# Kernel optimization log

Measured on AMD Instinct MI355X. Metric: run time of the kernel, lower is better.

Reference implementation:

```python
import jax, jax.numpy as jnp
import numpy as np

H, D = 4, 64          # n_heads, feats_per_head (hidden_size = H*D = 256)
NEG_SLOPE = 0.2       # DGL GATv2Conv default negative_slope

N_GT, N_UBS, N_AG = 100000, 20000, 20000
E_SEEN, E_NEAR = 320000, 160000
F_GT, F_UBS, F_AG = 8, 8, 16
HID = H * D


def _linear_params(key, fan_in, fan_out):
    kw, kb = jax.random.split(key)
    s = 1.0 / np.sqrt(fan_in)
    W = jax.random.uniform(kw, (fan_in, fan_out), jnp.float32, -s, s)
    b = jax.random.uniform(kb, (fan_out,), jnp.float32, -s, s)
    return W, b


def setup_inputs() -> dict:
    key = jax.random.key(0)
    ks = jax.random.split(key, 16)
    inp = {
        'x_gt': jax.random.normal(ks[0], (N_GT, F_GT), jnp.float32),
        'x_ubs': jax.random.normal(ks[1], (N_UBS, F_UBS), jnp.float32),
        'x_agent': jax.random.normal(ks[2], (N_AG, F_AG), jnp.float32),
        'seen_src': jax.random.randint(ks[3], (E_SEEN,), 0, N_GT, jnp.int32),
        'seen_dst': jax.random.randint(ks[4], (E_SEEN,), 0, N_AG, jnp.int32),
        'near_src': jax.random.randint(ks[5], (E_NEAR,), 0, N_UBS, jnp.int32),
        'near_dst': jax.random.randint(ks[6], (E_NEAR,), 0, N_AG, jnp.int32),
    }
    # GATv2Conv 'seen': (gt -> agent)
    inp['Ws_seen'], inp['bs_seen'] = _linear_params(ks[7], F_GT, HID)
    inp['Wd_seen'], inp['bd_seen'] = _linear_params(ks[8], F_AG, HID)
    inp['attn_seen'] = jax.random.normal(ks[9], (H, D), jnp.float32) * 0.1
    inp['Wr_seen'], inp['br_seen'] = _linear_params(ks[10], F_AG, HID)
    # GATv2Conv 'near': (ubs -> agent)
    inp['Ws_near'], inp['bs_near'] = _linear_params(ks[11], F_UBS, HID)
    inp['Wd_near'], inp['bd_near'] = _linear_params(ks[12], F_AG, HID)
    inp['attn_near'] = jax.random.normal(ks[13], (H, D), jnp.float32) * 0.1
    inp['Wr_near'], inp['br_near'] = _linear_params(ks[14], F_AG, HID)
    # aggregation MLP: Linear(2*HID, HID) + ReLU
    inp['W_aggr'], inp['b_aggr'] = _linear_params(ks[15], 2 * HID, HID)
    return inp


def _gatv2(h_src, h_dst, src, dst, Ws, bs, Wd, bd, attn, Wr, br, n_dst):
    # DGL GATv2Conv, bipartite, residual=True, allow_zero_in_degree, ReLU activation
    fs = (h_src @ Ws + bs).reshape(-1, H, D)   # [Ns,H,D]
    fd = (h_dst @ Wd + bd).reshape(-1, H, D)   # [Nd,H,D]
    e = jax.nn.leaky_relu(fs[src] + fd[dst], NEG_SLOPE)     # [E,H,D]
    scores = jnp.einsum('ehd,hd->eh', e, attn)              # [E,H]
    # edge softmax over incoming edges of each dst node
    m = jax.ops.segment_max(scores, dst, num_segments=n_dst)
    m = jnp.where(jnp.isfinite(m), m, 0.0)                  # zero-in-degree guard
    ex = jnp.exp(scores - m[dst])
    denom = jax.ops.segment_sum(ex, dst, num_segments=n_dst)
    alpha = ex / denom[dst]                                 # [E,H]
    rst = jax.ops.segment_sum(alpha[:, :, None] * fs[src], dst, num_segments=n_dst)
    rst = rst + (h_dst @ Wr + br).reshape(-1, H, D)         # residual
    return jax.nn.relu(rst).reshape(n_dst, H * D)


def reference(x_gt, x_ubs, x_agent, seen_src, seen_dst, near_src, near_dst,
              Ws_seen, bs_seen, Wd_seen, bd_seen, attn_seen, Wr_seen, br_seen,
              Ws_near, bs_near, Wd_near, bd_near, attn_near, Wr_near, br_near,
              W_aggr, b_aggr):
    n_ag = x_agent.shape[0]
    x1 = _gatv2(x_gt, x_agent, seen_src, seen_dst,
                Ws_seen, bs_seen, Wd_seen, bd_seen, attn_seen, Wr_seen, br_seen, n_ag)
    x2 = _gatv2(x_ubs, x_agent, near_src, near_dst,
                Ws_near, bs_near, Wd_near, bd_near, attn_near, Wr_near, br_near, n_ag)
    x_out = jnp.concatenate((x1, x2), axis=1)               # [N_ag, 2*HID]
    return jax.nn.relu(x_out @ W_aggr + b_aggr)             # [N_ag, HID]
```

## Files before the change

### kernel.cpp

```cpp
#include <hip/hip_runtime.h>
#include <math.h>

#define NEG 0.2f

typedef short bf16x8 __attribute__((ext_vector_type(8)));
typedef float f32x4  __attribute__((ext_vector_type(4)));
typedef float f32x2  __attribute__((ext_vector_type(2)));

static __device__ __forceinline__ void fma4(float4& d, float s, const float4 w) {
    d.x = fmaf(s, w.x, d.x); d.y = fmaf(s, w.y, d.y);
    d.z = fmaf(s, w.z, d.z); d.w = fmaf(s, w.w, d.w);
}
static __device__ __forceinline__ f32x2 pkfma(f32x2 a, f32x2 b, f32x2 c) {
    return __builtin_elementwise_fma(a, b, c);
}
static __device__ __forceinline__ f32x2 splat2(float x) { return (f32x2){x, x}; }

static __device__ __forceinline__ unsigned short f2bf(float f) {
    unsigned int x = __float_as_uint(f);
    unsigned int r = (x + 0x7FFFu + ((x >> 16) & 1u)) >> 16;
    return (unsigned short)r;
}
static __device__ __forceinline__ float rlane(float v, int l) {
    return __int_as_float(__builtin_amdgcn_readlane(__float_as_int(v), l));
}

#define DPP_ADD(x, ctrl) \
    ((x) + __int_as_float(__builtin_amdgcn_update_dpp( \
        __float_as_int(x), __float_as_int(x), (ctrl), 0xF, 0xF, true)))
static __device__ __forceinline__ float rowsum16(float v) {
    v = DPP_ADD(v, 0xB1);
    v = DPP_ADD(v, 0x4E);
    v = DPP_ADD(v, 0x141);
    v = DPP_ADD(v, 0x140);
    return v;
}

__global__ void k_hist_wt(const int* __restrict__ dst_s, int Es,
                          const int* __restrict__ dst_n, int En,
                          int* __restrict__ deg_s, int* __restrict__ deg_n,
                          const float* __restrict__ W, unsigned short* __restrict__ Wt) {
    int i = blockIdx.x * 256 + threadIdx.x;
    if (i < Es) atomicAdd(&deg_s[dst_s[i]], 1);
    int j = i - Es;
    if (j >= 0 && j < En) atomicAdd(&deg_n[dst_n[j]], 1);
    if (i < 512 * 256) {
        int k = i >> 8, n = i & 255;
        Wt[(size_t)n * 512 + k] = f2bf(W[i]);
    }
}

__global__ __launch_bounds__(1024) void k_scan2(int* a, int na, int* b, int nb) {
    int* p = (blockIdx.x == 0) ? a : b;
    int n  = (blockIdx.x == 0) ? na : nb;
    __shared__ int sums[1024];
    int t = threadIdx.x;
    int C = (n + 1023) >> 10;
    int base = t * C;
    int s = 0;
    for (int j = 0; j < C; ++j) { int i = base + j; if (i < n) s += p[i]; }
    sums[t] = s;
    __syncthreads();
    for (int off = 1; off < 1024; off <<= 1) {
        int v = (t >= off) ? sums[t - off] : 0;
        __syncthreads();
        sums[t] += v;
        __syncthreads();
    }
    int run = (t == 0) ? 0 : sums[t - 1];
    for (int j = 0; j < C; ++j) {
        int i = base + j;
        if (i < n) { int v = p[i]; p[i] = run; run += v; }
    }
}

__global__ void k_scatter(const int* __restrict__ src_s, const int* __restrict__ dst_s, int Es,
                          const int* __restrict__ src_n, const int* __restrict__ dst_n, int En,
                          int* __restrict__ cur_s, int* __restrict__ cur_n,
                          int* __restrict__ csr_s, int* __restrict__ csr_n) {
    int i = blockIdx.x * 256 + threadIdx.x;
    if (i < Es) {
        int pos = atomicAdd(&cur_s[dst_s[i]], 1);
        csr_s[pos] = src_s[i];
    }
    int j = i - Es;
    if (j >= 0 && j < En) {
        int pos = atomicAdd(&cur_n[dst_n[j]], 1);
        csr_n[pos] = src_n[j];
    }
}

__global__ __launch_bounds__(256) void k_gat(
    const float* __restrict__ xsrc_s, const int* __restrict__ pfx_s, const int* __restrict__ csr_s,
    const float* __restrict__ Ws_s, const float* __restrict__ bs_s,
    const float* __restrict__ Wd_s, const float* __restrict__ bd_s,
    const float* __restrict__ at_s,
    const float* __restrict__ Wr_s, const float* __restrict__ br_s,
    const float* __restrict__ xsrc_n, const int* __restrict__ pfx_n, const int* __restrict__ csr_n,
    const float* __restrict__ Ws_n, const float* __restrict__ bs_n,
    const float* __restrict__ Wd_n, const float* __restrict__ bd_n,
    const float* __restrict__ at_n,
    const float* __restrict__ Wr_n, const float* __restrict__ br_n,
    const float* __restrict__ x_ag,
    unsigned short* __restrict__ xcat, int n_dst, int gNs)
{
    const bool seen = (int)blockIdx.x < gNs;
    const float* x_src = seen ? xsrc_s : xsrc_n;
    const int*   pfx   = seen ? pfx_s  : pfx_n;
    const int*   csr   = seen ? csr_s  : csr_n;
    const float* Ws    = seen ? Ws_s   : Ws_n;
    const float* bs    = seen ? bs_s   : bs_n;
    const float* Wd    = seen ? Wd_s   : Wd_n;
    const float* bd    = seen ? bd_s   : bd_n;
    const float* at    = seen ? at_s   : at_n;
    const float* Wr    = seen ? Wr_s   : Wr_n;
    const float* br    = seen ? br_s   : br_n;
    const int col = seen ? 0 : 256;
    const int blk = seen ? (int)blockIdx.x : (int)blockIdx.x - gNs;

    const int t = threadIdx.x;
    const int wave = t >> 6, lane = t & 63;
    const int d0 = lane * 4;

    int gnode = blk * 16 + ((lane >> 4) << 2) + wave;
    int gn = (gnode < n_dst) ? gnode : (n_dst - 1);
    float xag = x_ag[(size_t)gn * 16 + (lane & 15)];

    int e_start[4], e_end[4];
#pragma unroll
    for (int j = 0; j < 4; ++j) {
        int nd = blk * 16 + j * 4 + wave;
        nd = (nd < n_dst) ? nd : (n_dst - 1);
        e_end[j]   = pfx[nd];
        e_start[j] = nd ? pfx[nd - 1] : 0;
    }

    f32x2 fd01[4], fd23[4], fr01[4], fr23[4];
    {
        float4 bdv = *(const float4*)&bd[d0];
        float4 brv = *(const float4*)&br[d0];
#pragma unroll
        for (int j = 0; j < 4; ++j) {
            fd01[j] = (f32x2){bdv.x, bdv.y}; fd23[j] = (f32x2){bdv.z, bdv.w};
            fr01[j] = (f32x2){brv.x, brv.y}; fr23[j] = (f32x2){brv.z, brv.w};
        }
#pragma unroll
        for (int k = 0; k < 16; ++k) {
            float4 wd = *(const float4*)&Wd[k * 256 + d0];
            float4 wr = *(const float4*)&Wr[k * 256 + d0];
            f32x2 wd01 = {wd.x, wd.y}, wd23 = {wd.z, wd.w};
            f32x2 wr01 = {wr.x, wr.y}, wr23 = {wr.z, wr.w};
#pragma unroll
            for (int j = 0; j < 4; ++j) {
                f32x2 xk = splat2(rlane(xag, j * 16 + k));
                fd01[j] = pkfma(xk, wd01, fd01[j]);
                fd23[j] = pkfma(xk, wd23, fd23[j]);
                fr01[j] = pkfma(xk, wr01, fr01[j]);
                fr23[j] = pkfma(xk, wr23, fr23[j]);
            }
        }
    }

    f32x2 ws01[8], ws23[8];
#pragma unroll
    for (int k = 0; k < 8; ++k) {
        float4 w = *(const float4*)&Ws[k * 256 + d0];
        ws01[k] = (f32x2){w.x, w.y};
        ws23[k] = (f32x2){w.z, w.w};
    }
    f32x2 bs01, bs23, at01, at23;
    {
        float4 b4 = *(const float4*)&bs[d0];
        float4 a4 = *(const float4*)&at[d0];
        bs01 = (f32x2){b4.x, b4.y}; bs23 = (f32x2){b4.z, b4.w};
        at01 = (f32x2){a4.x, a4.y}; at23 = (f32x2){a4.z, a4.w};
    }

#pragma unroll
    for (int rep = 0; rep < 4; ++rep) {
        const int node = blk * 16 + rep * 4 + wave;
        if (node >= n_dst) continue;

        const int start = e_start[rep];
        const int deg   = e_end[rep] - start;
        const f32x2 fd01r = fd01[rep], fd23r = fd23[rep];

        float l = 0.f;
        f32x2 a01 = {0.f, 0.f}, a23 = {0.f, 0.f};

        if (deg > 0) {
            const int gs = lane >> 3;
            const int w8 = lane & 7;

            int e0 = (gs < deg) ? gs : deg - 1;
            int i0 = csr[start + e0];
            float r0 = x_src[(size_t)i0 * 8 + w8];
            int e1 = (8 + gs < deg) ? 8 + gs : deg - 1;
            int i1 = csr[start + e1];

            for (int base = 0; base < deg; base += 8) {
                float r1 = x_src[(size_t)i1 * 8 + w8];
                int e2 = base + 16 + gs; e2 = (e2 < deg) ? e2 : deg - 1;
                int i2 = csr[start + e2];

#pragma unroll
                for (int j = 0; j < 8; ++j) {
                    if (base + j < deg) {
                        f32x2 x0 = splat2(rlane(r0, j * 8 + 0));
                        f32x2 x1 = splat2(rlane(r0, j * 8 + 1));
                        f32x2 x2 = splat2(rlane(r0, j * 8 + 2));
                        f32x2 x3 = splat2(rlane(r0, j * 8 + 3));
                        f32x2 x4 = splat2(rlane(r0, j * 8 + 4));
                        f32x2 x5 = splat2(rlane(r0, j * 8 + 5));
                        f32x2 x6 = splat2(rlane(r0, j * 8 + 6));
                        f32x2 x7 = splat2(rlane(r0, j * 8 + 7));

                        f32x2 fs01 = bs01, fs23 = bs23;
                        fs01 = pkfma(x0, ws01[0], fs01); fs23 = pkfma(x0, ws23[0], fs23);
                        fs01 = pkfma(x1, ws01[1], fs01); fs23 = pkfma(x1, ws23[1], fs23);
                        fs01 = pkfma(x2, ws01[2], fs01); fs23 = pkfma(x2, ws23[2], fs23);
                        fs01 = pkfma(x3, ws01[3], fs01); fs23 = pkfma(x3, ws23[3], fs23);
                        fs01 = pkfma(x4, ws01[4], fs01); fs23 = pkfma(x4, ws23[4], fs23);
                        fs01 = pkfma(x5, ws01[5], fs01); fs23 = pkfma(x5, ws23[5], fs23);
                        fs01 = pkfma(x6, ws01[6], fs01); fs23 = pkfma(x6, ws23[6], fs23);
                        fs01 = pkfma(x7, ws01[7], fs01); fs23 = pkfma(x7, ws23[7], fs23);

                        f32x2 t01 = fs01 + fd01r;
                        f32x2 t23 = fs23 + fd23r;
                        t01 = __builtin_elementwise_max(t01, NEG * t01);
                        t23 = __builtin_elementwise_max(t23, NEG * t23);

                        f32x2 scp = t01 * at01;
                        scp = pkfma(t23, at23, scp);
                        float sc = scp.x + scp.y;
                        sc = rowsum16(sc);

                        float p = __expf(sc);
                        l += p;
                        f32x2 pp = splat2(p);
                        a01 = pkfma(pp, fs01, a01);
                        a23 = pkfma(pp, fs23, a23);
                    }
                }
                r0 = r1; i1 = i2;
            }
        }

        float inv = (l > 0.f) ? 1.f / l : 0.f;
        ushort4 o;
        o.x = f2bf(fmaxf(fmaf(a01.x, inv, fr01[rep].x), 0.f));
        o.y = f2bf(fmaxf(fmaf(a01.y, inv, fr01[rep].y), 0.f));
        o.z = f2bf(fmaxf(fmaf(a23.x, inv, fr23[rep].x), 0.f));
        o.w = f2bf(fmaxf(fmaf(a23.y, inv, fr23[rep].y), 0.f));
        *(ushort4*)&xcat[(size_t)node * 512 + col + d0] = o;
    }
}

__global__ __launch_bounds__(256) void k_mlp(
    const unsigned short* __restrict__ X, const unsigned short* __restrict__ Wt,
    const float* __restrict__ b, float* __restrict__ out, int M)
{
    const int t = threadIdx.x;
    const int wave = t >> 6, lane = t & 63;
    const int m16 = lane & 15, q = lane >> 4;
    const int rbase = blockIdx.x * 16;
    const int nbase = wave * 64;

    int rowa = rbase + m16; if (rowa >= M) rowa = M - 1;
    const unsigned short* xp = X + (size_t)rowa * 512 + q * 8;
    const unsigned short* w0 = Wt + (size_t)(nbase + m16) * 512 + q * 8;
    const unsigned short* w1 = w0 + 16 * 512;
    const unsigned short* w2 = w0 + 32 * 512;
    const unsigned short* w3 = w0 + 48 * 512;

    f32x4 ac0 = {0.f, 0.f, 0.f, 0.f}, ac1 = ac0, ac2 = ac0, ac3 = ac0;

#pragma unroll
    for (int k0 = 0; k0 < 512; k0 += 32) {
        bf16x8 a  = *(const bf16x8*)(xp + k0);
        bf16x8 b0 = *(const bf16x8*)(w0 + k0);
        bf16x8 b1 = *(const bf16x8*)(w1 + k0);
        bf16x8 b2 = *(const bf16x8*)(w2 + k0);
        bf16x8 b3 = *(const bf16x8*)(w3 + k0);
        ac0 = __builtin_amdgcn_mfma_f32_16x16x32_bf16(a, b0, ac0, 0, 0, 0);
        ac1 = __builtin_amdgcn_mfma_f32_16x16x32_bf16(a, b1, ac1, 0, 0, 0);
        ac2 = __builtin_amdgcn_mfma_f32_16x16x32_bf16(a, b2, ac2, 0, 0, 0);
        ac3 = __builtin_amdgcn_mfma_f32_16x16x32_bf16(a, b3, ac3, 0, 0, 0);
    }

#define EPI(AC, J) { \
        int coln = nbase + (J) * 16 + m16; \
        float bias = b[coln]; \
        _Pragma("unroll") \
        for (int r = 0; r < 4; ++r) { \
            int orow = rbase + q * 4 + r; \
            if (orow < M) \
                out[(size_t)orow * 256 + coln] = fmaxf(AC[r] + bias, 0.f); \
        } }
    EPI(ac0, 0) EPI(ac1, 1) EPI(ac2, 2) EPI(ac3, 3)
#undef EPI
}

extern "C" void kernel_launch(void* const* d_in, const int* in_sizes, int n_in,
                              void* d_out, int out_size, void* d_ws, size_t ws_size,
                              hipStream_t stream) {
    const float* x_gt   = (const float*)d_in[0];
    const float* x_ubs  = (const float*)d_in[1];
    const float* x_ag   = (const float*)d_in[2];
    const int* seen_src = (const int*)d_in[3];
    const int* seen_dst = (const int*)d_in[4];
    const int* near_src = (const int*)d_in[5];
    const int* near_dst = (const int*)d_in[6];
    const float* Ws_s = (const float*)d_in[7];  const float* bs_s = (const float*)d_in[8];
    const float* Wd_s = (const float*)d_in[9];  const float* bd_s = (const float*)d_in[10];
    const float* at_s = (const float*)d_in[11];
    const float* Wr_s = (const float*)d_in[12]; const float* br_s = (const float*)d_in[13];
    const float* Ws_n = (const float*)d_in[14]; const float* bs_n = (const float*)d_in[15];
    const float* Wd_n = (const float*)d_in[16]; const float* bd_n = (const float*)d_in[17];
    const float* at_n = (const float*)d_in[18];
    const float* Wr_n = (const float*)d_in[19]; const float* br_n = (const float*)d_in[20];
    const float* W_a  = (const float*)d_in[21]; const float* b_a  = (const float*)d_in[22];

    const int n_ag = in_sizes[2] / 16;
    const int E_s  = in_sizes[3];
    const int E_n  = in_sizes[5];

    char* ws = (char*)d_ws;
    int* cur_s = (int*)ws;              ws += (size_t)n_ag * 4;
    int* cur_n = (int*)ws;              ws += (size_t)n_ag * 4;
    int* csr_s = (int*)ws;              ws += (size_t)E_s * 4;
    int* csr_n = (int*)ws;              ws += (size_t)E_n * 4;
    unsigned short* xcat = (unsigned short*)ws;  ws += (size_t)n_ag * 512 * 2;
    unsigned short* Wt   = (unsigned short*)ws;

    hipMemsetAsync(cur_s, 0, (size_t)n_ag * 8, stream);

    int gE = (E_s + E_n + 255) / 256;
    k_hist_wt<<<gE, 256, 0, stream>>>(seen_dst, E_s, near_dst, E_n, cur_s, cur_n, W_a, Wt);
    k_scan2<<<2, 1024, 0, stream>>>(cur_s, n_ag, cur_n, n_ag);
    k_scatter<<<gE, 256, 0, stream>>>(seen_src, seen_dst, E_s, near_src, near_dst, E_n,
                                      cur_s, cur_n, csr_s, csr_n);

    int gN = (n_ag + 15) / 16;
    k_gat<<<2 * gN, 256, 0, stream>>>(
        x_gt,  cur_s, csr_s, Ws_s, bs_s, Wd_s, bd_s, at_s, Wr_s, br_s,
        x_ubs, cur_n, csr_n, Ws_n, bs_n, Wd_n, bd_n, at_n, Wr_n, br_n,
        x_ag, xcat, n_ag, gN);

    k_mlp<<<(n_ag + 15) / 16, 256, 0, stream>>>(xcat, Wt, b_a, (float*)d_out, n_ag);
}
```

Measured before the change: 310.5 us.

## Fuse GATv2 layers and aggregation MLP into one kernel via LDS staging

Merges the two GATv2 passes and the MLP into one 512-thread kernel. Each block handles 16 destination nodes with both edge types and stages the bf16 concatenated features in padded shared memory, which the MFMA GEMM then reads directly. This drops the xcat global round trip and one launch, and prefetches the first edge indices before each layer. The cost is that each wave now runs both layers serially, the grid has half as many blocks, the block is larger, and per-thread register pressure rises.

```diff
diff --git a/kernel.cpp b/kernel.cpp
--- a/kernel.cpp
+++ b/kernel.cpp
@@ -2,15 +2,12 @@
 #include <math.h>
 
 #define NEG 0.2f
+#define LDSW 520
 
 typedef short bf16x8 __attribute__((ext_vector_type(8)));
 typedef float f32x4  __attribute__((ext_vector_type(4)));
 typedef float f32x2  __attribute__((ext_vector_type(2)));
 
-static __device__ __forceinline__ void fma4(float4& d, float s, const float4 w) {
-    d.x = fmaf(s, w.x, d.x); d.y = fmaf(s, w.y, d.y);
-    d.z = fmaf(s, w.z, d.z); d.w = fmaf(s, w.w, d.w);
-}
 static __device__ __forceinline__ f32x2 pkfma(f32x2 a, f32x2 b, f32x2 c) {
     return __builtin_elementwise_fma(a, b, c);
 }
@@ -90,7 +87,134 @@
     }
 }
 
-__global__ __launch_bounds__(256) void k_gat(
+#define EDGE_BODY { \
+    f32x2 x0 = splat2(rlane(r0, j * 8 + 0)); \
+    f32x2 x1 = splat2(rlane(r0, j * 8 + 1)); \
+    f32x2 x2 = splat2(rlane(r0, j * 8 + 2)); \
+    f32x2 x3 = splat2(rlane(r0, j * 8 + 3)); \
+    f32x2 x4 = splat2(rlane(r0, j * 8 + 4)); \
+    f32x2 x5 = splat2(rlane(r0, j * 8 + 5)); \
+    f32x2 x6 = splat2(rlane(r0, j * 8 + 6)); \
+    f32x2 x7 = splat2(rlane(r0, j * 8 + 7)); \
+    f32x2 fs01 = bs01, fs23 = bs23; \
+    fs01 = pkfma(x0, ws01[0], fs01); fs23 = pkfma(x0, ws23[0], fs23); \
+    fs01 = pkfma(x1, ws01[1], fs01); fs23 = pkfma(x1, ws23[1], fs23); \
+    fs01 = pkfma(x2, ws01[2], fs01); fs23 = pkfma(x2, ws23[2], fs23); \
+    fs01 = pkfma(x3, ws01[3], fs01); fs23 = pkfma(x3, ws23[3], fs23); \
+    fs01 = pkfma(x4, ws01[4], fs01); fs23 = pkfma(x4, ws23[4], fs23); \
+    fs01 = pkfma(x5, ws01[5], fs01); fs23 = pkfma(x5, ws23[5], fs23); \
+    fs01 = pkfma(x6, ws01[6], fs01); fs23 = pkfma(x6, ws23[6], fs23); \
+    fs01 = pkfma(x7, ws01[7], fs01); fs23 = pkfma(x7, ws23[7], fs23); \
+    f32x2 t01 = fs01 + fd01r; \
+    f32x2 t23 = fs23 + fd23r; \
+    t01 = __builtin_elementwise_max(t01, NEG * t01); \
+    t23 = __builtin_elementwise_max(t23, NEG * t23); \
+    f32x2 scp = t01 * at01; \
+    scp = pkfma(t23, at23, scp); \
+    float sc = scp.x + scp.y; \
+    sc = rowsum16(sc); \
+    float p = __expf(sc);    \
+    l += p; \
+    f32x2 pp = splat2(p); \
+    a01 = pkfma(pp, fs01, a01); \
+    a23 = pkfma(pp, fs23, a23); }
+
+static __device__ __forceinline__ void gat_layer(
+    const float* __restrict__ x_src, const int* __restrict__ csr,
+    const float* __restrict__ Ws, const float* __restrict__ bs,
+    const float* __restrict__ Wd, const float* __restrict__ bd,
+    const float* __restrict__ at,
+    const float* __restrict__ Wr, const float* __restrict__ br,
+    float xag, int lane,
+    const int* st, const int* dg,
+    const int* i1pre, const float* x0pre,
+    unsigned short* __restrict__ ldsout)
+{
+    const int d0 = lane * 4;
+    const int gs = lane >> 3;
+    const int w8 = lane & 7;
+
+    f32x2 fd01[2], fd23[2], fr01[2], fr23[2];
+    {
+        float4 bdv = *(const float4*)&bd[d0];
+        float4 brv = *(const float4*)&br[d0];
+#pragma unroll
+        for (int j = 0; j < 2; ++j) {
+            fd01[j] = (f32x2){bdv.x, bdv.y}; fd23[j] = (f32x2){bdv.z, bdv.w};
+            fr01[j] = (f32x2){brv.x, brv.y}; fr23[j] = (f32x2){brv.z, brv.w};
+        }
+#pragma unroll
+        for (int k = 0; k < 16; ++k) {
+            float4 wd = *(const float4*)&Wd[k * 256 + d0];
+            float4 wr = *(const float4*)&Wr[k * 256 + d0];
+            f32x2 wd01 = {wd.x, wd.y}, wd23 = {wd.z, wd.w};
+            f32x2 wr01 = {wr.x, wr.y}, wr23 = {wr.z, wr.w};
+#pragma unroll
+            for (int j = 0; j < 2; ++j) {
+                f32x2 xk = splat2(rlane(xag, j * 16 + k));
+                fd01[j] = pkfma(xk, wd01, fd01[j]);
+                fd23[j] = pkfma(xk, wd23, fd23[j]);
+                fr01[j] = pkfma(xk, wr01, fr01[j]);
+                fr23[j] = pkfma(xk, wr23, fr23[j]);
+            }
+        }
+    }
+
+    f32x2 ws01[8], ws23[8];
+#pragma unroll
+    for (int k = 0; k < 8; ++k) {
+        float4 w = *(const float4*)&Ws[k * 256 + d0];
+        ws01[k] = (f32x2){w.x, w.y};
+        ws23[k] = (f32x2){w.z, w.w};
+    }
+    f32x2 bs01, bs23, at01, at23;
+    {
+        float4 b4 = *(const float4*)&bs[d0];
+        float4 a4 = *(const float4*)&at[d0];
+        bs01 = (f32x2){b4.x, b4.y}; bs23 = (f32x2){b4.z, b4.w};
+        at01 = (f32x2){a4.x, a4.y}; at23 = (f32x2){a4.z, a4.w};
+    }
+
+#pragma unroll
+    for (int rep = 0; rep < 2; ++rep) {
+        const int start = st[rep];
+        const int deg   = dg[rep];
+        const f32x2 fd01r = fd01[rep], fd23r = fd23[rep];
+
+        float l = 0.f;
+        f32x2 a01 = {0.f, 0.f}, a23 = {0.f, 0.f};
+
+        if (deg > 0) {
+            float r0 = x0pre[rep];
+            int   i1 = i1pre[rep];
+            const int nfull = deg >> 3, tail = deg & 7;
+
+            for (int c = 0; c < nfull; ++c) {
+                float r1 = x_src[(size_t)i1 * 8 + w8];
+                int e2 = c * 8 + 16 + gs; e2 = (e2 < deg) ? e2 : deg - 1;
+                int i2 = csr[start + e2];
+#pragma unroll
+                for (int j = 0; j < 8; ++j) EDGE_BODY
+                r0 = r1; i1 = i2;
+            }
+            if (tail) {
+#pragma unroll
+                for (int j = 0; j < 8; ++j)
+                    if (j < tail) EDGE_BODY
+            }
+        }
+
+        float inv = (l > 0.f) ? 1.f / l : 0.f;
+        ushort4 o;
+        o.x = f2bf(fmaxf(fmaf(a01.x, inv, fr01[rep].x), 0.f));
+        o.y = f2bf(fmaxf(fmaf(a01.y, inv, fr01[rep].y), 0.f));
+        o.z = f2bf(fmaxf(fmaf(a23.x, inv, fr23[rep].x), 0.f));
+        o.w = f2bf(fmaxf(fmaf(a23.y, inv, fr23[rep].y), 0.f));
+        *(ushort4*)(ldsout + rep * LDSW) = o;
+    }
+}
+
+__global__ __launch_bounds__(512) void k_gatmlp(
     const float* __restrict__ xsrc_s, const int* __restrict__ pfx_s, const int* __restrict__ csr_s,
     const float* __restrict__ Ws_s, const float* __restrict__ bs_s,
     const float* __restrict__ Wd_s, const float* __restrict__ bd_s,
@@ -102,202 +226,95 @@
     const float* __restrict__ at_n,
     const float* __restrict__ Wr_n, const float* __restrict__ br_n,
     const float* __restrict__ x_ag,
-    unsigned short* __restrict__ xcat, int n_dst, int gNs)
+    const unsigned short* __restrict__ Wt, const float* __restrict__ bmlp,
+    float* __restrict__ out, int n_dst)
 {
-    const bool seen = (int)blockIdx.x < gNs;
-    const float* x_src = seen ? xsrc_s : xsrc_n;
-    const int*   pfx   = seen ? pfx_s  : pfx_n;
-    const int*   csr   = seen ? csr_s  : csr_n;
-    const float* Ws    = seen ? Ws_s   : Ws_n;
-    const float* bs    = seen ? bs_s   : bs_n;
-    const float* Wd    = seen ? Wd_s   : Wd_n;
-    const float* bd    = seen ? bd_s   : bd_n;
-    const float* at    = seen ? at_s   : at_n;
-    const float* Wr    = seen ? Wr_s   : Wr_n;
-    const float* br    = seen ? br_s   : br_n;
-    const int col = seen ? 0 : 256;
-    const int blk = seen ? (int)blockIdx.x : (int)blockIdx.x - gNs;
+    __shared__ unsigned short xt[16 * LDSW];
 
     const int t = threadIdx.x;
     const int wave = t >> 6, lane = t & 63;
-    const int d0 = lane * 4;
-
-    int gnode = blk * 16 + ((lane >> 4) << 2) + wave;
-    int gn = (gnode < n_dst) ? gnode : (n_dst - 1);
-    float xag = x_ag[(size_t)gn * 16 + (lane & 15)];
-
-    int e_start[4], e_end[4];
-#pragma unroll
-    for (int j = 0; j < 4; ++j) {
-        int nd = blk * 16 + j * 4 + wave;
-        nd = (nd < n_dst) ? nd : (n_dst - 1);
-        e_end[j]   = pfx[nd];
-        e_start[j] = nd ? pfx[nd - 1] : 0;
-    }
-
-    f32x2 fd01[4], fd23[4], fr01[4], fr23[4];
-    {
-        float4 bdv = *(const float4*)&bd[d0];
-        float4 brv = *(const float4*)&br[d0];
-#pragma unroll
-        for (int j = 0; j < 4; ++j) {
-            fd01[j] = (f32x2){bdv.x, bdv.y}; fd23[j] = (f32x2){bdv.z, bdv.w};
-            fr01[j] = (f32x2){brv.x, brv.y}; fr23[j] = (f32x2){brv.z, brv.w};
-        }
-#pragma unroll
-        for (int k = 0; k < 16; ++k) {
-            float4 wd = *(const float4*)&Wd[k * 256 + d0];
-            float4 wr = *(const float4*)&Wr[k * 256 + d0];
-            f32x2 wd01 = {wd.x, wd.y}, wd23 = {wd.z, wd.w};
-            f32x2 wr01 = {wr.x, wr.y}, wr23 = {wr.z, wr.w};
-#pragma unroll
-            for (int j = 0; j < 4; ++j) {
-                f32x2 xk = splat2(rlane(xag, j * 16 + k));
-                fd01[j] = pkfma(xk, wd01, fd01[j]);
-                fd23[j] = pkfma(xk, wd23, fd23[j]);
-                fr01[j] = pkfma(xk, wr01, fr01[j]);
-                fr23[j] = pkfma(xk, wr23, fr23[j]);
-            }
-        }
-    }
-
-    f32x2 ws01[8], ws23[8];
-#pragma unroll
-    for (int k = 0; k < 8; ++k) {
-        float4 w = *(const float4*)&Ws[k * 256 + d0];
-        ws01[k] = (f32x2){w.x, w.y};
-        ws23[k] = (f32x2){w.z, w.w};
-    }
-    f32x2 bs01, bs23, at01, at23;
-    {
-        float4 b4 = *(const float4*)&bs[d0];
-        float4 a4 = *(const float4*)&at[d0];
-        bs01 = (f32x2){b4.x, b4.y}; bs23 = (f32x2){b4.z, b4.w};
-        at01 = (f32x2){a4.x, a4.y}; at23 = (f32x2){a4.z, a4.w};
-    }
-
-#pragma unroll
-    for (int rep = 0; rep < 4; ++rep) {
-        const int node = blk * 16 + rep * 4 + wave;
-        if (node >= n_dst) continue;
-
-        const int start = e_start[rep];
-        const int deg   = e_end[rep] - start;
-        const f32x2 fd01r = fd01[rep], fd23r = fd23[rep];
-
-        float l = 0.f;
-        f32x2 a01 = {0.f, 0.f}, a23 = {0.f, 0.f};
-
-        if (deg > 0) {
-            const int gs = lane >> 3;
-            const int w8 = lane & 7;
-
-            int e0 = (gs < deg) ? gs : deg - 1;
-            int i0 = csr[start + e0];
-            float r0 = x_src[(size_t)i0 * 8 + w8];
-            int e1 = (8 + gs < deg) ? 8 + gs : deg - 1;
-            int i1 = csr[start + e1];
-
-            for (int base = 0; base < deg; base += 8) {
-                float r1 = x_src[(size_t)i1 * 8 + w8];
-                int e2 = base + 16 + gs; e2 = (e2 < deg) ? e2 : deg - 1;
-                int i2 = csr[start + e2];
-
-#pragma unroll
-                for (int j = 0; j < 8; ++j) {
-                    if (base + j < deg) {
-                        f32x2 x0 = splat2(rlane(r0, j * 8 + 0));
-                        f32x2 x1 = splat2(rlane(r0, j * 8 + 1));
-                        f32x2 x2 = splat2(rlane(r0, j * 8 + 2));
-                        f32x2 x3 = splat2(rlane(r0, j * 8 + 3));
-                        f32x2 x4 = splat2(rlane(r0, j * 8 + 4));
-                        f32x2 x5 = splat2(rlane(r0, j * 8 + 5));
-                        f32x2 x6 = splat2(rlane(r0, j * 8 + 6));
-                        f32x2 x7 = splat2(rlane(r0, j * 8 + 7));
-
-                        f32x2 fs01 = bs01, fs23 = bs23;
-                        fs01 = pkfma(x0, ws01[0], fs01); fs23 = pkfma(x0, ws23[0], fs23);
-                        fs01 = pkfma(x1, ws01[1], fs01); fs23 = pkfma(x1, ws23[1], fs23);
-                        fs01 = pkfma(x2, ws01[2], fs01); fs23 = pkfma(x2, ws23[2], fs23);
-                        fs01 = pkfma(x3, ws01[3], fs01); fs23 = pkfma(x3, ws23[3], fs23);
-                        fs01 = pkfma(x4, ws01[4], fs01); fs23 = pkfma(x4, ws23[4], fs23);
-                        fs01 = pkfma(x5, ws01[5], fs01); fs23 = pkfma(x5, ws23[5], fs23);
-                        fs01 = pkfma(x6, ws01[6], fs01); fs23 = pkfma(x6, ws23[6], fs23);
-                        fs01 = pkfma(x7, ws01[7], fs01); fs23 = pkfma(x7, ws23[7], fs23);
-
-                        f32x2 t01 = fs01 + fd01r;
-                        f32x2 t23 = fs23 + fd23r;
-                        t01 = __builtin_elementwise_max(t01, NEG * t01);
-                        t23 = __builtin_elementwise_max(t23, NEG * t23);
-
-                        f32x2 scp = t01 * at01;
-                        scp = pkfma(t23, at23, scp);
-                        float sc = scp.x + scp.y;
-                        sc = rowsum16(sc);
-
-                        float p = __expf(sc);
-                        l += p;
-                        f32x2 pp = splat2(p);
-                        a01 = pkfma(pp, fs01, a01);
-                        a23 = pkfma(pp, fs23, a23);
-                    }
-                }
-                r0 = r1; i1 = i2;
-            }
-        }
-
-        float inv = (l > 0.f) ? 1.f / l : 0.f;
-        ushort4 o;
-        o.x = f2bf(fmaxf(fmaf(a01.x, inv, fr01[rep].x), 0.f));
-        o.y = f2bf(fmaxf(fmaf(a01.y, inv, fr01[rep].y), 0.f));
-        o.z = f2bf(fmaxf(fmaf(a23.x, inv, fr23[rep].x), 0.f));
-        o.w = f2bf(fmaxf(fmaf(a23.y, inv, fr23[rep].y), 0.f));
-        *(ushort4*)&xcat[(size_t)node * 512 + col + d0] = o;
-    }
-}
-
-__global__ __launch_bounds__(256) void k_mlp(
-    const unsigned short* __restrict__ X, const unsigned short* __restrict__ Wt,
-    const float* __restrict__ b, float* __restrict__ out, int M)
-{
-    const int t = threadIdx.x;
-    const int wave = t >> 6, lane = t & 63;
+    const int gs = lane >> 3, w8 = lane & 7;
+    const int nb = (int)blockIdx.x * 16;
+
+    int nd0 = nb + wave * 2;     nd0 = (nd0 < n_dst) ? nd0 : n_dst - 1;
+    int nd1 = nb + wave * 2 + 1; nd1 = (nd1 < n_dst) ? nd1 : n_dst - 1;
+
+    float xag = x_ag[(size_t)(((lane >> 4) & 1) ? nd1 : nd0) * 16 + (lane & 15)];
+
+    int stS[2], dgS[2], stN[2], dgN[2];
+#pragma unroll
+    for (int j = 0; j < 2; ++j) {
+        int n = j ? nd1 : nd0;
+        int eS = pfx_s[n], sS = n ? pfx_s[n - 1] : 0;
+        int eN = pfx_n[n], sN = n ? pfx_n[n - 1] : 0;
+        stS[j] = sS; dgS[j] = eS - sS;
+        stN[j] = sN; dgN[j] = eN - sN;
+    }
+
+    int i0S[2], i1S[2]; float x0S[2];
+#pragma unroll
+    for (int j = 0; j < 2; ++j) {
+        int dgj = dgS[j];
+        if (dgj > 0) {
+            int e0 = (gs < dgj) ? gs : dgj - 1;
+            int e1 = (8 + gs < dgj) ? 8 + gs : dgj - 1;
+            i0S[j] = csr_s[stS[j] + e0];
+            i1S[j] = csr_s[stS[j] + e1];
+        } else { i0S[j] = 0; i1S[j] = 0; }
+    }
+#pragma unroll
+    for (int j = 0; j < 2; ++j)
+        x0S[j] = xsrc_s[(size_t)i0S[j] * 8 + w8];
+
+    unsigned short* ldsA = &xt[(wave * 2) * LDSW + lane * 4];
+    gat_layer(xsrc_s, csr_s, Ws_s, bs_s, Wd_s, bd_s, at_s, Wr_s, br_s,
+              xag, lane, stS, dgS, i1S, x0S, ldsA);
+
+    int i0N[2], i1N[2]; float x0N[2];
+#pragma unroll
+    for (int j = 0; j < 2; ++j) {
+        int dgj = dgN[j];
+        if (dgj > 0) {
+            int e0 = (gs < dgj) ? gs : dgj - 1;
+            int e1 = (8 + gs < dgj) ? 8 + gs : dgj - 1;
+            i0N[j] = csr_n[stN[j] + e0];
+            i1N[j] = csr_n[stN[j] + e1];
+        } else { i0N[j] = 0; i1N[j] = 0; }
+    }
+#pragma unroll
+    for (int j = 0; j < 2; ++j)
+        x0N[j] = xsrc_n[(size_t)i0N[j] * 8 + w8];
+
+    gat_layer(xsrc_n, csr_n, Ws_n, bs_n, Wd_n, bd_n, at_n, Wr_n, br_n,
+              xag, lane, stN, dgN, i1N, x0N, ldsA + 256);
+
+    __syncthreads();
+
     const int m16 = lane & 15, q = lane >> 4;
-    const int rbase = blockIdx.x * 16;
-    const int nbase = wave * 64;
-
-    int rowa = rbase + m16; if (rowa >= M) rowa = M - 1;
-    const unsigned short* xp = X + (size_t)rowa * 512 + q * 8;
-    const unsigned short* w0 = Wt + (size_t)(nbase + m16) * 512 + q * 8;
+    const unsigned short* w0 = Wt + (size_t)(wave * 32 + m16) * 512 + q * 8;
     const unsigned short* w1 = w0 + 16 * 512;
-    const unsigned short* w2 = w0 + 32 * 512;
-    const unsigned short* w3 = w0 + 48 * 512;
-
-    f32x4 ac0 = {0.f, 0.f, 0.f, 0.f}, ac1 = ac0, ac2 = ac0, ac3 = ac0;
-
+    const unsigned short* ap = &xt[m16 * LDSW + q * 8];
+
+    f32x4 ac0 = {0.f, 0.f, 0.f, 0.f}, ac1 = ac0;
 #pragma unroll
     for (int k0 = 0; k0 < 512; k0 += 32) {
-        bf16x8 a  = *(const bf16x8*)(xp + k0);
+        bf16x8 a  = *(const bf16x8*)(ap + k0);
         bf16x8 b0 = *(const bf16x8*)(w0 + k0);
         bf16x8 b1 = *(const bf16x8*)(w1 + k0);
-        bf16x8 b2 = *(const bf16x8*)(w2 + k0);
-        bf16x8 b3 = *(const bf16x8*)(w3 + k0);
         ac0 = __builtin_amdgcn_mfma_f32_16x16x32_bf16(a, b0, ac0, 0, 0, 0);
         ac1 = __builtin_amdgcn_mfma_f32_16x16x32_bf16(a, b1, ac1, 0, 0, 0);
-        ac2 = __builtin_amdgcn_mfma_f32_16x16x32_bf16(a, b2, ac2, 0, 0, 0);
-        ac3 = __builtin_amdgcn_mfma_f32_16x16x32_bf16(a, b3, ac3, 0, 0, 0);
     }
 
 #define EPI(AC, J) { \
-        int coln = nbase + (J) * 16 + m16; \
-        float bias = b[coln]; \
+        int coln = wave * 32 + (J) * 16 + m16; \
+        float bv = bmlp[coln]; \
         _Pragma("unroll") \
         for (int r = 0; r < 4; ++r) { \
-            int orow = rbase + q * 4 + r; \
-            if (orow < M) \
-                out[(size_t)orow * 256 + coln] = fmaxf(AC[r] + bias, 0.f); \
+            int orow = nb + q * 4 + r; \
+            if (orow < n_dst) \
+                out[(size_t)orow * 256 + coln] = fmaxf(AC[r] + bv, 0.f); \
         } }
-    EPI(ac0, 0) EPI(ac1, 1) EPI(ac2, 2) EPI(ac3, 3)
+    EPI(ac0, 0) EPI(ac1, 1)
 #undef EPI
 }
 
@@ -330,7 +347,6 @@
     int* cur_n = (int*)ws;              ws += (size_t)n_ag * 4;
     int* csr_s = (int*)ws;              ws += (size_t)E_s * 4;
     int* csr_n = (int*)ws;              ws += (size_t)E_n * 4;
-    unsigned short* xcat = (unsigned short*)ws;  ws += (size_t)n_ag * 512 * 2;
     unsigned short* Wt   = (unsigned short*)ws;
 
     hipMemsetAsync(cur_s, 0, (size_t)n_ag * 8, stream);
@@ -342,10 +358,8 @@
                                       cur_s, cur_n, csr_s, csr_n);
 
     int gN = (n_ag + 15) / 16;
-    k_gat<<<2 * gN, 256, 0, stream>>>(
+    k_gatmlp<<<gN, 512, 0, stream>>>(
         x_gt,  cur_s, csr_s, Ws_s, bs_s, Wd_s, bd_s, at_s, Wr_s, br_s,
         x_ubs, cur_n, csr_n, Ws_n, bs_n, Wd_n, bd_n, at_n, Wr_n, br_n,
-        x_ag, xcat, n_ag, gN);
-
-    k_mlp<<<(n_ag + 15) / 16, 256, 0, stream>>>(xcat, Wt, b_a, (float*)d_out, n_ag);
-}
+        x_ag, Wt, b_a, (float*)d_out, n_ag);
+}
```

Result: no change. 311.1 us (+0.2%).
